# Kernel tuning notes

Hardware: AMD Instinct MI355X
Metric: run time of the kernel (lower is better)

## Reference

```python
import jax, jax.numpy as jnp
import numpy as np

NUM_RELATIONS = 3
NUM_HEADS = 1

N_NODES = 50000
N_EDGES = 300000
D = 256  # in_channels == out_channels == out_channels*num_heads
W_SCALE = 0.02  # realistic init scale; keeps linear-attention normalizer dominated by N_r


def setup_inputs() -> dict:
    key = jax.random.key(0)
    k = jax.random.split(key, 7)
    x = jax.random.normal(k[0], (N_NODES, D), dtype=jnp.float32)
    Wq = jax.random.normal(k[1], (NUM_RELATIONS, D, D * NUM_HEADS), dtype=jnp.float32) * W_SCALE
    Wk = jax.random.normal(k[2], (NUM_RELATIONS, D, D * NUM_HEADS), dtype=jnp.float32) * W_SCALE
    Wv = jax.random.normal(k[3], (NUM_RELATIONS, D, D * NUM_HEADS), dtype=jnp.float32) * W_SCALE
    Whp = jax.random.normal(k[4], (D * NUM_HEADS, D), dtype=jnp.float32) * W_SCALE
    edge_index = jax.random.randint(k[5], (2, N_EDGES), 0, N_NODES, dtype=jnp.int64)
    edge_type = jax.random.randint(k[6], (N_EDGES,), 0, NUM_RELATIONS, dtype=jnp.int64)
    return {"x": x, "Wq": Wq, "Wk": Wk, "Wv": Wv, "Whp": Whp,
            "edge_index": edge_index, "edge_type": edge_type}


def _trans_conv(x, Wq, Wk, Wv, Whp, edge_index, edge_type):
    # x: [N, F], Wq/Wk/Wv: [R, F, H*Dh], Whp: [H*Dh, Dh], edge_index: [2, E]
    row, col = edge_index[0], edge_index[1]
    N = x.shape[0]
    R = Wq.shape[0]
    H = NUM_HEADS
    Dh = Wq.shape[-1] // H
    xr = x[row]  # [E, F] gathered source-node features
    xc = x[col]  # [E, F] gathered target-node features
    x_out = jnp.zeros((N, Dh), dtype=x.dtype)
    for r in range(R):  # small fixed relation loop (structurally distinct weights)
        m = (edge_type == r).astype(x.dtype)  # [E] relation mask (handles ragged sizes)
        Nr = jnp.sum(m)  # number of edges of this relation (the 'N' in full_attention_conv)
        q = (xr @ Wq[r]).reshape(-1, H, Dh)  # [E, H, Dh]
        kk = (xc @ Wk[r]).reshape(-1, H, Dh)
        v = (xc @ Wv[r]).reshape(-1, H, Dh)
        # linear attention (no softmax), masked so only relation-r edges contribute
        kvs = jnp.einsum('e,ehm,ehd->hmd', m, kk, v)        # [H, Dh, Dh]
        num = jnp.einsum('ehm,hmd->ehd', q, kvs) + Nr * v    # [E, H, Dh]
        ks_sum = jnp.einsum('e,ehm->hm', m, kk)              # [H, Dh]
        norm = jnp.einsum('ehm,hm->eh', q, ks_sum)[..., None] + Nr  # [E, H, 1]
        attn = (num / norm).mean(axis=1)                     # [E, Dh] (mean over heads)
        x_out = x_out.at[row].add(m[:, None] * attn)         # scatter-add to source nodes
    return x_out @ Whp  # head projection


def reference(x, Wq, Wk, Wv, Whp, edge_index, edge_type):
    return _trans_conv(x, Wq, Wk, Wv, Whp, edge_index, edge_type)
```

## Files before the change

kernel.cpp:

```cpp
#include <hip/hip_runtime.h>

#define NN 50000
#define EE 300000
#define DD 256
#define RR 3
#define NPAD 50048
#define GS 64
#define SCT (RR * NN)
#define SCB 1024
#define SNB ((SCT + SCB - 1) / SCB)
#define TBLK 3128

using bf16x8 = __attribute__((ext_vector_type(8))) short;
using f32x4  = __attribute__((ext_vector_type(4))) float;

__device__ __forceinline__ float bf2f(unsigned short u) {
    return __uint_as_float(((unsigned)u) << 16);
}
__device__ __forceinline__ unsigned short f2bf(float f) {
    unsigned u = __float_as_uint(f);
    return (unsigned short)((u + 0x7fffu + ((u >> 16) & 1u)) >> 16);
}
__device__ __forceinline__ void gload_lds16(const void* g, void* l) {
    __builtin_amdgcn_global_load_lds(
        (const __attribute__((address_space(1))) unsigned int*)g,
        (__attribute__((address_space(3))) unsigned int*)l, 16, 0, 0);
}

__global__ __launch_bounds__(256) void prep_tc(
    const float* __restrict__ x, const float* __restrict__ Wq,
    const float* __restrict__ Wk, const float* __restrict__ Wv,
    const float* __restrict__ Whp,
    unsigned short* __restrict__ xb, unsigned short* __restrict__ xT,
    unsigned short* __restrict__ Wqb, unsigned short* __restrict__ Wkb,
    unsigned short* __restrict__ Wvb, unsigned short* __restrict__ WhpT)
{
    const int tid = threadIdx.x;
    if (blockIdx.x < TBLK) {
        __shared__ unsigned short t[64][66];
        const int tb = blockIdx.x;
        const int n0 = (tb % 782) * 64, i0 = (tb / 782) * 64;
        const int nl = tid >> 2, c0 = (tid & 3) * 16;
        unsigned short vb[16];
        int n = n0 + nl;
        if (n < NN) {
            const float* src = x + (size_t)n * DD + i0 + c0;
#pragma unroll
            for (int q = 0; q < 16; q += 4) {
                float4 v = *(const float4*)(src + q);
                vb[q] = f2bf(v.x); vb[q + 1] = f2bf(v.y);
                vb[q + 2] = f2bf(v.z); vb[q + 3] = f2bf(v.w);
            }
#pragma unroll
            for (int q = 0; q < 16; q += 4)
                *(ushort4*)(xb + (size_t)n * DD + i0 + c0 + q) =
                    make_ushort4(vb[q], vb[q + 1], vb[q + 2], vb[q + 3]);
        } else {
#pragma unroll
            for (int q = 0; q < 16; q++) vb[q] = 0;
        }
#pragma unroll
        for (int q = 0; q < 16; q++) t[nl][c0 + q] = vb[q];
        __syncthreads();
        const int il = tid >> 2, nc0 = (tid & 3) * 16;
        unsigned short ob[16];
#pragma unroll
        for (int q = 0; q < 16; q++) ob[q] = t[nc0 + q][il];
#pragma unroll
        for (int q = 0; q < 16; q += 4)
            *(ushort4*)(xT + (size_t)(i0 + il) * NPAD + n0 + nc0 + q) =
                make_ushort4(ob[q], ob[q + 1], ob[q + 2], ob[q + 3]);
    } else {
        int t = (blockIdx.x - TBLK) * 256 + tid;
        int slot = t >> 16, o = t & 65535;
        int a = o >> 8, b = o & 255;
        if (slot < 3)       Wqb[(size_t)slot * 65536 + o] = f2bf(Wq[(size_t)slot * 65536 + o]);
        else if (slot < 6)  Wkb[(size_t)(slot - 3) * 65536 + o] = f2bf(Wk[(size_t)(slot - 3) * 65536 + o]);
        else if (slot < 9)  Wvb[(size_t)(slot - 6) * 65536 + o] = f2bf(Wv[(size_t)(slot - 6) * 65536 + o]);
        else if (slot == 9) WhpT[o] = f2bf(Whp[b * 256 + a]);
    }
}

__global__ __launch_bounds__(256) void count_kernel(
    const int* __restrict__ erow, const int* __restrict__ ecol,
    const int* __restrict__ etype, int* __restrict__ c_in,
    int* __restrict__ c_out, int* __restrict__ nr)
{
    __shared__ int lnr[RR];
    if (threadIdx.x < RR) lnr[threadIdx.x] = 0;
    __syncthreads();
    int g = blockIdx.x * blockDim.x + threadIdx.x;
    int stride = gridDim.x * blockDim.x;
    for (int e = g; e < EE; e += stride) {
        int t = etype[e];
        atomicAdd(&c_out[t * NN + erow[e]], 1);
        atomicAdd(&c_in[t * NN + ecol[e]], 1);
        atomicAdd(&lnr[t], 1);
    }
    __syncthreads();
    if (threadIdx.x < RR) atomicAdd(&nr[threadIdx.x], lnr[threadIdx.x]);
}

__global__ __launch_bounds__(256) void scan_reduce(
    const int* __restrict__ cnt, int* __restrict__ bsum)
{
    __shared__ int ws[4];
    const int b = blockIdx.x, tid = threadIdx.x;
    const int i = b * SCB + tid * 4;
    int s = 0;
    if (i < SCT) {
        int4 v = *(const int4*)(cnt + i);
        s = v.x + v.y + v.z + v.w;
    }
#pragma unroll
    for (int off = 32; off; off >>= 1) s += __shfl_down(s, off, 64);
    if ((tid & 63) == 0) ws[tid >> 6] = s;
    __syncthreads();
    if (tid == 0) bsum[b] = ws[0] + ws[1] + ws[2] + ws[3];
}

__global__ __launch_bounds__(256) void scan_top(
    const int* __restrict__ bsum, int* __restrict__ boff, int* __restrict__ offT)
{
    __shared__ int bs[256];
    const int tid = threadIdx.x;
    int v = tid < SNB ? bsum[tid] : 0;
    bs[tid] = v;
    __syncthreads();
    for (int d = 1; d < 256; d <<= 1) {
        int t = (tid >= d) ? bs[tid - d] : 0;
        __syncthreads();
        bs[tid] += t;
        __syncthreads();
    }
    if (tid < SNB) boff[tid] = tid ? bs[tid - 1] : 0;
    if (tid == 255) *offT = bs[255];
}

__global__ __launch_bounds__(256) void scan_bot(
    const int* __restrict__ cnt, const int* __restrict__ boff,
    int* __restrict__ off, int* __restrict__ cur)
{
    __shared__ int bs[256];
    const int b = blockIdx.x, tid = threadIdx.x;
    const int i = b * SCB + tid * 4;
    int4 v = make_int4(0, 0, 0, 0);
    if (i < SCT) v = *(const int4*)(cnt + i);
    int s = v.x + v.y + v.z + v.w;
    bs[tid] = s;
    __syncthreads();
    for (int d = 1; d < 256; d <<= 1) {
        int t = (tid >= d) ? bs[tid - d] : 0;
        __syncthreads();
        bs[tid] += t;
        __syncthreads();
    }
    if (i < SCT) {
        int pre = boff[b] + (tid ? bs[tid - 1] : 0);
        int4 o;
        o.x = pre;
        o.y = pre + v.x;
        o.z = pre + v.x + v.y;
        o.w = pre + v.x + v.y + v.z;
        *(int4*)(off + i) = o;
        *(int4*)(cur + i) = o;
    }
}

__global__ __launch_bounds__(256) void fill_kernel(
    const int* __restrict__ erow, const int* __restrict__ ecol,
    const int* __restrict__ etype, int* __restrict__ cur,
    int* __restrict__ scol)
{
    int e = blockIdx.x * 256 + threadIdx.x;
    if (e < EE) {
        int key = etype[e] * NN + erow[e];
        int p = atomicAdd(&cur[key], 1);
        scol[p] = ecol[e];
    }
}

__global__ __launch_bounds__(256) void wbfxw_kernel(
    const unsigned short* __restrict__ xT, const int* __restrict__ c_in,
    float* __restrict__ xw, unsigned short* __restrict__ wbf)
{
    const int tid = threadIdx.x;
    if (blockIdx.x < 256) {
        __shared__ float red[3][4];
        const int i = blockIdx.x;
        float a0 = 0.f, a1 = 0.f, a2 = 0.f;
        for (int n = tid * 4; n < NN; n += 1024) {
            ushort4 xv = *(const ushort4*)(xT + (size_t)i * NPAD + n);
            int4 w0 = *(const int4*)(c_in + n);
            int4 w1 = *(const int4*)(c_in + NN + n);
            int4 w2 = *(const int4*)(c_in + 2 * NN + n);
            float f0 = bf2f(xv.x), f1 = bf2f(xv.y), f2 = bf2f(xv.z), f3 = bf2f(xv.w);
            a0 += f0 * w0.x + f1 * w0.y + f2 * w0.z + f3 * w0.w;
            a1 += f0 * w1.x + f1 * w1.y + f2 * w1.z + f3 * w1.w;
            a2 += f0 * w2.x + f1 * w2.y + f2 * w2.z + f3 * w2.w;
        }
#pragma unroll
        for (int off = 32; off; off >>= 1) {
            a0 += __shfl_down(a0, off, 64);
            a1 += __shfl_down(a1, off, 64);
            a2 += __shfl_down(a2, off, 64);
        }
        if ((tid & 63) == 0) {
            red[0][tid >> 6] = a0; red[1][tid >> 6] = a1; red[2][tid >> 6] = a2;
        }
        __syncthreads();
        if (tid < 3)
            xw[tid * 256 + i] = red[tid][0] + red[tid][1] + red[tid][2] + red[tid][3];
    } else {
        int t = (blockIdx.x - 256) * 256 + tid;
        if (t < 3 * NPAD) {
            int r = t / NPAD, n = t % NPAD;
            wbf[t] = f2bf(n < NN ? (float)c_in[r * NN + n] : 0.f);
        }
    }
}

__global__ __launch_bounds__(512) void g_kernel(
    const unsigned short* __restrict__ xT, const unsigned short* __restrict__ wbf,
    float* __restrict__ Gp)
{
    __shared__ __align__(16) char ldsA[16384];
    __shared__ __align__(16) char ldsB[16384];
    const int tid = threadIdx.x, lane = tid & 63, wid = tid >> 6;
    const int wr = wid >> 1, wc = wid & 1;
    const int i0 = blockIdx.x * 128, j0 = blockIdx.y * 128;
    const int TPZ = (NPAD / 64 + GS - 1) / GS;
    const int kt0 = blockIdx.z * TPZ;
    const int kt1 = min(NPAD / 64, kt0 + TPZ);

    f32x4 acc[3][2][4];
#pragma unroll
    for (int r = 0; r < 3; r++)
#pragma unroll
        for (int m = 0; m < 2; m++)
#pragma unroll
            for (int n = 0; n < 4; n++) acc[r][m][n] = (f32x4){0.f, 0.f, 0.f, 0.f};

    for (int kt = kt0; kt < kt1; kt++) {
        const int kbyte = kt * 128;
#pragma unroll
        for (int is = 0; is < 2; is++) {
            int lb = is * 8192 + wid * 1024;
            int d = lb + lane * 16;
            int row = d >> 7;
            int sc_ = (d & 127) ^ ((row & 7) << 4);
            gload_lds16((const char*)xT + (size_t)(i0 + row) * (NPAD * 2) + kbyte + sc_, ldsA + lb);
            gload_lds16((const char*)xT + (size_t)(j0 + row) * (NPAD * 2) + kbyte + sc_, ldsB + lb);
        }
        __syncthreads();
#pragma unroll
        for (int kk = 0; kk < 2; kk++) {
            const int cb = kk * 64 + ((lane >> 4) << 4);
            bf16x8 bfr[4];
#pragma unroll
            for (int n = 0; n < 4; n++) {
                int rn = wc * 64 + n * 16 + (lane & 15);
                bfr[n] = *(const bf16x8*)(ldsB + rn * 128 + (cb ^ ((rn & 7) << 4)));
            }
            float au[2][8];
#pragma unroll
            for (int m = 0; m < 2; m++) {
                int row = wr * 32 + m * 16 + (lane & 15);
                bf16x8 ar = *(const bf16x8*)(ldsA + row * 128 + (cb ^ ((row & 7) << 4)));
#pragma unroll
                for (int q = 0; q < 8; q++) au[m][q] = bf2f((unsigned short)ar[q]);
            }
            const int nb = kt * 64 + kk * 32 + ((lane >> 4) << 3);
#pragma unroll
            for (int r = 0; r < 3; r++) {
                bf16x8 wv = *(const bf16x8*)(wbf + (size_t)r * NPAD + nb);
                float wf[8];
#pragma unroll
                for (int q = 0; q < 8; q++) wf[q] = bf2f((unsigned short)wv[q]);
                bf16x8 am[2];
#pragma unroll
                for (int m = 0; m < 2; m++)
#pragma unroll
                    for (int q = 0; q < 8; q++)
                        am[m][q] = (short)f2bf(au[m][q] * wf[q]);
#pragma unroll
                for (int m = 0; m < 2; m++)
#pragma unroll
                    for (int n = 0; n < 4; n++)
                        acc[r][m][n] = __builtin_amdgcn_mfma_f32_16x16x32_bf16(
                            am[m], bfr[n], acc[r][m][n], 0, 0, 0);
            }
        }
        __syncthreads();
    }
    float* base = Gp + ((size_t)blockIdx.z * 4 + blockIdx.x * 2 + blockIdx.y) * 3 * 16384;
#pragma unroll
    for (int r = 0; r < 3; r++)
#pragma unroll
        for (int m = 0; m < 2; m++)
#pragma unroll
            for (int n = 0; n < 4; n++) {
                int col = wc * 64 + n * 16 + (lane & 15);
                int rw0 = wr * 32 + m * 16 + ((lane >> 4) << 2);
#pragma unroll
                for (int reg = 0; reg < 4; reg++)
                    base[r * 16384 + (rw0 + reg) * 128 + col] = acc[r][m][n][reg];
            }
}

__global__ __launch_bounds__(256) void greduce_kernel(
    const float* __restrict__ Gp, unsigned short* __restrict__ Gb)
{
    int gid = blockIdx.x * 256 + threadIdx.x;
    int t = gid >> 14, rem = gid & 16383;
    int r = t % 3, tile = t / 3;
    float s = 0.f;
    for (int z = 0; z < GS; z++)
        s += Gp[(size_t)z * 196608 + ((size_t)tile * 3 + r) * 16384 + rem];
    int i = (tile >> 1) * 128 + (rem >> 7);
    int j = (tile & 1) * 128 + (rem & 127);
    Gb[(size_t)r * 65536 + i * 256 + j] = f2bf(s);
}

__global__ __launch_bounds__(256) void matvec_bf(
    const unsigned short* __restrict__ Mat, const float* __restrict__ v,
    float* __restrict__ y)
{
    __shared__ float vs[256];
    const int b = blockIdx.x;
    const int r = b >> 6, rb = (b & 63) * 4;
    const int tid = threadIdx.x;
    vs[tid] = v[r * 256 + tid];
    __syncthreads();
    const int wid = tid >> 6, lane = tid & 63;
    const int row = rb + wid;
    ushort4 m4 = *(const ushort4*)(Mat + (size_t)r * 65536 + row * 256 + lane * 4);
    float s = bf2f(m4.x) * vs[lane * 4] + bf2f(m4.y) * vs[lane * 4 + 1] +
              bf2f(m4.z) * vs[lane * 4 + 2] + bf2f(m4.w) * vs[lane * 4 + 3];
#pragma unroll
    for (int off = 32; off; off >>= 1) s += __shfl_down(s, off, 64);
    if (lane == 0) y[r * 256 + row] = s;
}

__global__ __launch_bounds__(256) void gather_kernel(
    const unsigned short* __restrict__ xb, const int* __restrict__ scol,
    const int* __restrict__ off, const float* __restrict__ tv,
    const int* __restrict__ c_out, const int* __restrict__ nr,
    unsigned short* __restrict__ Afull)
{
    __shared__ float ts[768];
    __shared__ float nrs[RR];
    const int tid = threadIdx.x;
    for (int k = tid; k < 768; k += 256) ts[k] = tv[k];
    if (tid < RR) nrs[tid] = (float)nr[tid];
    __syncthreads();
    const int wid = tid >> 6, lane = tid & 63;
    const int n = blockIdx.x * 4 + wid;
    if (n >= NN) return;
    ushort4 xv = *(const ushort4*)(xb + (size_t)n * DD + lane * 4);
    float xf[4] = {bf2f(xv.x), bf2f(xv.y), bf2f(xv.z), bf2f(xv.w)};
    float dots[RR];
#pragma unroll
    for (int t = 0; t < RR; t++) {
        float s = xf[0] * ts[t * 256 + lane * 4] + xf[1] * ts[t * 256 + lane * 4 + 1] +
                  xf[2] * ts[t * 256 + lane * 4 + 2] + xf[3] * ts[t * 256 + lane * 4 + 3];
#pragma unroll
        for (int o = 32; o; o >>= 1) s += __shfl_xor(s, o, 64);
        dots[t] = s;
    }
#pragma unroll
    for (int t = 0; t < RR; t++) {
        float nrf = nrs[t];
        float denom = dots[t] + nrf;
        int cnt = c_out[t * NN + n];
        float s2 = cnt ? (float)cnt / denom : 0.f;
        ushort4 o1;
        o1.x = f2bf(s2 * xf[0]); o1.y = f2bf(s2 * xf[1]);
        o1.z = f2bf(s2 * xf[2]); o1.w = f2bf(s2 * xf[3]);
        *(ushort4*)(Afull + (size_t)n * 1536 + t * 256 + lane * 4) = o1;

        float acc[4] = {0.f, 0.f, 0.f, 0.f};
        int b0 = off[t * NN + n], b1 = off[t * NN + n + 1];
        for (int i = b0; i < b1; i++) {
            int col = scol[i];
            ushort4 v = *(const ushort4*)(xb + (size_t)col * DD + lane * 4);
            acc[0] += bf2f(v.x); acc[1] += bf2f(v.y);
            acc[2] += bf2f(v.z); acc[3] += bf2f(v.w);
        }
        float s1 = nrf / denom;
        ushort4 o2;
        o2.x = f2bf(s1 * acc[0]); o2.y = f2bf(s1 * acc[1]);
        o2.z = f2bf(s1 * acc[2]); o2.w = f2bf(s1 * acc[3]);
        *(ushort4*)(Afull + (size_t)n * 1536 + 768 + t * 256 + lane * 4) = o2;
    }
}

template <int MODE, int SWZ>
__global__ __launch_bounds__(256) void gemm_nt(
    const unsigned short* __restrict__ A, int lda,
    const unsigned short* __restrict__ B, int ldb,
    void* __restrict__ Cv, int ldc, int M, int KK,
    size_t sa, size_t sb, size_t sc)
{
    A += (size_t)blockIdx.z * sa;
    B += (size_t)blockIdx.z * sb;
    __shared__ __align__(16) char ldsA[16384];
    __shared__ __align__(16) char ldsB[16384];
    const int tid = threadIdx.x, lane = tid & 63, wid = tid >> 6;
    const int wr = wid >> 1, wc = wid & 1;
    int bx = blockIdx.x;
    if (SWZ) {
        int nwg = gridDim.x, q = nwg >> 3, rem = nwg & 7;
        int xcd = bx & 7, idx = bx >> 3;
        bx = (xcd < rem ? xcd * (q + 1) : rem * (q + 1) + (xcd - rem) * q) + idx;
    }
    const int row0 = bx * 128, col0 = blockIdx.y * 128;

    f32x4 acc[4][4];
#pragma unroll
    for (int m = 0; m < 4; m++)
#pragma unroll
        for (int n = 0; n < 4; n++) acc[m][n] = (f32x4){0.f, 0.f, 0.f, 0.f};

    for (int k0 = 0; k0 < KK; k0 += 64) {
#pragma unroll
        for (int is = 0; is < 4; is++) {
            int lb = is * 4096 + wid * 1024;
            int d = lb + lane * 16;
            int row = d >> 7;
            int sc_ = (d & 127) ^ ((row & 7) << 4);
            int gr = row0 + row; gr = gr < M ? gr : M - 1;
            gload_lds16((const char*)(A + (size_t)gr * lda + k0) + sc_, ldsA + lb);
            int rn = col0 + row;
            gload_lds16((const char*)(B + (size_t)rn * ldb + k0) + sc_, ldsB + lb);
        }
        __syncthreads();
#pragma unroll
        for (int kk = 0; kk < 2; kk++) {
            bf16x8 af[4], bf_[4];
            const int cb = kk * 64 + ((lane >> 4) << 4);
#pragma unroll
            for (int m = 0; m < 4; m++) {
                int row = wr * 64 + m * 16 + (lane & 15);
                af[m] = *(const bf16x8*)(ldsA + row * 128 + (cb ^ ((row & 7) << 4)));
                int rn = wc * 64 + m * 16 + (lane & 15);
                bf_[m] = *(const bf16x8*)(ldsB + rn * 128 + (cb ^ ((rn & 7) << 4)));
            }
#pragma unroll
            for (int m = 0; m < 4; m++)
#pragma unroll
                for (int n = 0; n < 4; n++)
                    acc[m][n] = __builtin_amdgcn_mfma_f32_16x16x32_bf16(
                        af[m], bf_[n], acc[m][n], 0, 0, 0);
        }
        __syncthreads();
    }

#pragma unroll
    for (int m = 0; m < 4; m++) {
#pragma unroll
        for (int reg = 0; reg < 4; reg++) {
            int r = row0 + wr * 64 + m * 16 + ((lane >> 4) << 2) + reg;
            if (r >= M) continue;
#pragma unroll
            for (int n = 0; n < 4; n++) {
                int c = col0 + wc * 64 + n * 16 + (lane & 15);
                float v = acc[m][n][reg];
                if (MODE == 0)
                    ((unsigned short*)Cv)[(size_t)blockIdx.z * sc + (size_t)r * ldc + c] = f2bf(v);
                else
                    ((float*)Cv)[(size_t)blockIdx.z * sc + (size_t)r * ldc + c] = v;
            }
        }
    }
}

extern "C" void kernel_launch(void* const* d_in, const int* in_sizes, int n_in,
                              void* d_out, int out_size, void* d_ws, size_t ws_size,
                              hipStream_t stream)
{
    const float* x   = (const float*)d_in[0];
    const float* Wq  = (const float*)d_in[1];
    const float* Wk  = (const float*)d_in[2];
    const float* Wv  = (const float*)d_in[3];
    const float* Whp = (const float*)d_in[4];
    const int* eidx  = (const int*)d_in[5];
    const int* etyp  = (const int*)d_in[6];
    const int* erow = eidx;
    const int* ecol = eidx + EE;
    float* out = (float*)d_out;

    char* p = (char*)d_ws;
    unsigned short* xb    = (unsigned short*)p; p += (size_t)NN * DD * 2;
    unsigned short* xT    = (unsigned short*)p; p += (size_t)DD * NPAD * 2;
    char*           regB  = p;                  p += (size_t)NN * 1536 * 2;
    unsigned short* Gb    = (unsigned short*)p; p += (size_t)RR * 65536 * 2;
    unsigned short* M1    = (unsigned short*)p; p += (size_t)RR * 65536 * 2;
    unsigned short* Tm    = (unsigned short*)p; p += (size_t)RR * 65536 * 2;
    unsigned short* Bout  = (unsigned short*)p; p += (size_t)256 * 1536 * 2;
    unsigned short* Wqb   = (unsigned short*)p; p += (size_t)RR * 65536 * 2;
    unsigned short* Wkb   = (unsigned short*)p; p += (size_t)RR * 65536 * 2;
    unsigned short* Wvb   = (unsigned short*)p; p += (size_t)RR * 65536 * 2;
    unsigned short* WhpT  = (unsigned short*)p; p += 65536 * 2;
    unsigned short* wbf   = (unsigned short*)p; p += (size_t)RR * NPAD * 2;
    float*          xw    = (float*)p;          p += 768 * 4;
    float*          tv    = (float*)p;          p += 768 * 4;
    int*            c_in  = (int*)p;            p += (size_t)RR * NN * 4;
    int*            c_out = (int*)p;            p += (size_t)RR * NN * 4;
    int*            nr    = (int*)p;            p += 4 * 4;
    int*            off   = (int*)p;            p += (size_t)(RR * NN + 4) * 4;
    int*            cur   = (int*)p;            p += (size_t)RR * NN * 4;
    int*            scol  = (int*)p;            p += (size_t)EE * 4;
    int*            bsum  = (int*)p;            p += SNB * 4;
    int*            boff  = (int*)p;            p += SNB * 4;
    float*          Gp    = (float*)regB;
    unsigned short* Afull = (unsigned short*)regB;

    prep_tc<<<TBLK + 2560, 256, 0, stream>>>(x, Wq, Wk, Wv, Whp, xb, xT, Wqb, Wkb, Wvb, WhpT);
    hipMemsetAsync(c_in, 0, (size_t)(6 * NN + 4) * sizeof(int), stream);
    count_kernel<<<512, 256, 0, stream>>>(erow, ecol, etyp, c_in, c_out, nr);
    scan_reduce<<<SNB, 256, 0, stream>>>(c_out, bsum);
    scan_top<<<1, 256, 0, stream>>>(bsum, boff, off + SCT);
    scan_bot<<<SNB, 256, 0, stream>>>(c_out, boff, off, cur);
    fill_kernel<<<(EE + 255) / 256, 256, 0, stream>>>(erow, ecol, etyp, cur, scol);
    wbfxw_kernel<<<256 + (3 * NPAD + 255) / 256, 256, 0, stream>>>(xT, c_in, xw, wbf);

    gemm_nt<0, 0><<<dim3(2, 2, 3), 256, 0, stream>>>(Wqb, 256, Wkb, 256, M1, 256, 256, 256,
                                                     65536, 65536, 65536);
    gemm_nt<0, 0><<<dim3(2, 2, 3), 256, 0, stream>>>(WhpT, 256, Wvb, 256, Bout + 768, 1536,
                                                     256, 256, 0, 65536, 256);

    g_kernel<<<dim3(2, 2, GS), 512, 0, stream>>>(xT, wbf, Gp);
    greduce_kernel<<<12 * 64, 256, 0, stream>>>(Gp, Gb);

    gemm_nt<0, 0><<<dim3(2, 2, 3), 256, 0, stream>>>(M1, 256, Gb, 256, Tm, 256, 256, 256,
                                                     65536, 65536, 65536);
    gemm_nt<0, 0><<<dim3(2, 2, 3), 256, 0, stream>>>(Bout + 768, 1536, Tm, 256, Bout, 1536,
                                                     256, 256, 256, 65536, 256);
    matvec_bf<<<192, 256, 0, stream>>>(M1, xw, tv);

    gather_kernel<<<(NN + 3) / 4, 256, 0, stream>>>(xb, scol, off, tv, c_out, nr, Afull);

    const int MB = (NN + 127) / 128;
    gemm_nt<1, 1><<<dim3(MB, 2), 256, 0, stream>>>(Afull, 1536, Bout, 1536, out, 256, NN, 1536,
                                                   0, 0, 0);
}
```

Baseline: 320.2 us.

## Replace final projection GEMM with 256x256-tile 1024-thread double-buffered kernel

```diff
diff --git a/kernel.cpp b/kernel.cpp
--- a/kernel.cpp
+++ b/kernel.cpp
@@ -470,6 +470,96 @@
                     ((unsigned short*)Cv)[(size_t)blockIdx.z * sc + (size_t)r * ldc + c] = f2bf(v);
                 else
                     ((float*)Cv)[(size_t)blockIdx.z * sc + (size_t)r * ldc + c] = v;
+            }
+        }
+    }
+}
+
+__global__ __launch_bounds__(1024) void gemm_big(
+    const unsigned short* __restrict__ A, int lda,
+    const unsigned short* __restrict__ B, int ldb,
+    float* __restrict__ C, int ldc, int M, int KK)
+{
+    extern __shared__ __align__(16) char lds[];
+    char* ldsA = lds;
+    char* ldsB = lds + 65536;
+    const int tid = threadIdx.x, lane = tid & 63, wid = tid >> 6;
+    const int wr = wid >> 2, wc = wid & 3;
+    int bx = blockIdx.x;
+    {
+        int nwg = gridDim.x, q = nwg >> 3, rem = nwg & 7;
+        int xcd = bx & 7, idx = bx >> 3;
+        bx = (xcd < rem ? xcd * (q + 1) : rem * (q + 1) + (xcd - rem) * q) + idx;
+    }
+    const int row0 = bx * 256, col0 = blockIdx.y * 256;
+
+    f32x4 acc[4][4];
+#pragma unroll
+    for (int m = 0; m < 4; m++)
+#pragma unroll
+        for (int n = 0; n < 4; n++) acc[m][n] = (f32x4){0.f, 0.f, 0.f, 0.f};
+
+    const int NT = KK / 64;
+    int cur = 0;
+
+#define STAGE_TILE(buf, t)                                                     \
+    {                                                                          \
+        const int k0_ = (t) * 64;                                              \
+        _Pragma("unroll")                                                      \
+        for (int is = 0; is < 2; is++) {                                       \
+            int lb = is * 16384 + wid * 1024;                                  \
+            int d = lb + lane * 16;                                            \
+            int row = d >> 7;                                                  \
+            int sc_ = (d & 127) ^ ((row & 7) << 4);                            \
+            int gr = row0 + row; gr = gr < M ? gr : M - 1;                     \
+            gload_lds16((const char*)(A + (size_t)gr * lda + k0_) + sc_,       \
+                        ldsA + (buf) * 32768 + lb);                            \
+            int rn = col0 + row;                                               \
+            gload_lds16((const char*)(B + (size_t)rn * ldb + k0_) + sc_,       \
+                        ldsB + (buf) * 32768 + lb);                            \
+        }                                                                      \
+    }
+
+    STAGE_TILE(0, 0);
+    __syncthreads();
+
+    for (int t = 0; t < NT; t++) {
+        if (t + 1 < NT) STAGE_TILE(cur ^ 1, t + 1);
+        const char* bA = ldsA + cur * 32768;
+        const char* bB = ldsB + cur * 32768;
+#pragma unroll
+        for (int kk = 0; kk < 2; kk++) {
+            bf16x8 af[4], bf_[4];
+            const int cb = kk * 64 + ((lane >> 4) << 4);
+#pragma unroll
+            for (int m = 0; m < 4; m++) {
+                int row = wr * 64 + m * 16 + (lane & 15);
+                af[m] = *(const bf16x8*)(bA + row * 128 + (cb ^ ((row & 7) << 4)));
+                int rn = wc * 64 + m * 16 + (lane & 15);
+                bf_[m] = *(const bf16x8*)(bB + rn * 128 + (cb ^ ((rn & 7) << 4)));
+            }
+#pragma unroll
+            for (int m = 0; m < 4; m++)
+#pragma unroll
+                for (int n = 0; n < 4; n++)
+                    acc[m][n] = __builtin_amdgcn_mfma_f32_16x16x32_bf16(
+                        af[m], bf_[n], acc[m][n], 0, 0, 0);
+        }
+        __syncthreads();
+        cur ^= 1;
+    }
+#undef STAGE_TILE
+
+#pragma unroll
+    for (int m = 0; m < 4; m++) {
+#pragma unroll
+        for (int reg = 0; reg < 4; reg++) {
+            int r = row0 + wr * 64 + m * 16 + ((lane >> 4) << 2) + reg;
+            if (r >= M) continue;
+#pragma unroll
+            for (int n = 0; n < 4; n++) {
+                int c = col0 + wc * 64 + n * 16 + (lane & 15);
+                C[(size_t)r * ldc + c] = acc[m][n][reg];
             }
         }
     }
@@ -516,6 +606,9 @@
     float*          Gp    = (float*)regB;
     unsigned short* Afull = (unsigned short*)regB;
 
+    hipFuncSetAttribute((const void*)gemm_big,
+                        hipFuncAttributeMaxDynamicSharedMemorySize, 131072);
+
     prep_tc<<<TBLK + 2560, 256, 0, stream>>>(x, Wq, Wk, Wv, Whp, xb, xT, Wqb, Wkb, Wvb, WhpT);
     hipMemsetAsync(c_in, 0, (size_t)(6 * NN + 4) * sizeof(int), stream);
     count_kernel<<<512, 256, 0, stream>>>(erow, ecol, etyp, c_in, c_out, nr);
@@ -541,7 +634,6 @@
 
     gather_kernel<<<(NN + 3) / 4, 256, 0, stream>>>(xb, scol, off, tv, c_out, nr, Afull);
 
-    const int MB = (NN + 127) / 128;
-    gemm_nt<1, 1><<<dim3(MB, 2), 256, 0, stream>>>(Afull, 1536, Bout, 1536, out, 256, NN, 1536,
-                                                   0, 0, 0);
-}
+    const int MB2 = (NN + 255) / 256;
+    gemm_big<<<dim3(MB2, 1), 1024, 131072, stream>>>(Afull, 1536, Bout, 1536, out, 256, NN, 1536);
+}
```

After: 292.1 us. 8.8% less time.

## Fuse per-row scaled x blocks into final GEMM instead of materializing them

Applied to the files above, without the earlier changes.

```diff
diff --git a/kernel.cpp b/kernel.cpp
--- a/kernel.cpp
+++ b/kernel.cpp
@@ -346,7 +346,7 @@
     const unsigned short* __restrict__ xb, const int* __restrict__ scol,
     const int* __restrict__ off, const float* __restrict__ tv,
     const int* __restrict__ c_out, const int* __restrict__ nr,
-    unsigned short* __restrict__ Afull)
+    unsigned short* __restrict__ Ascat, float* __restrict__ s2g)
 {
     __shared__ float ts[768];
     __shared__ float nrs[RR];
@@ -372,13 +372,10 @@
     for (int t = 0; t < RR; t++) {
         float nrf = nrs[t];
         float denom = dots[t] + nrf;
-        int cnt = c_out[t * NN + n];
-        float s2 = cnt ? (float)cnt / denom : 0.f;
-        ushort4 o1;
-        o1.x = f2bf(s2 * xf[0]); o1.y = f2bf(s2 * xf[1]);
-        o1.z = f2bf(s2 * xf[2]); o1.w = f2bf(s2 * xf[3]);
-        *(ushort4*)(Afull + (size_t)n * 1536 + t * 256 + lane * 4) = o1;
-
+        if (lane == 0) {
+            int cnt = c_out[t * NN + n];
+            s2g[(size_t)t * NN + n] = cnt ? (float)cnt / denom : 0.f;
+        }
         float acc[4] = {0.f, 0.f, 0.f, 0.f};
         int b0 = off[t * NN + n], b1 = off[t * NN + n + 1];
         for (int i = b0; i < b1; i++) {
@@ -391,7 +388,7 @@
         ushort4 o2;
         o2.x = f2bf(s1 * acc[0]); o2.y = f2bf(s1 * acc[1]);
         o2.z = f2bf(s1 * acc[2]); o2.w = f2bf(s1 * acc[3]);
-        *(ushort4*)(Afull + (size_t)n * 1536 + 768 + t * 256 + lane * 4) = o2;
+        *(ushort4*)(Ascat + (size_t)n * 768 + t * 256 + lane * 4) = o2;
     }
 }
 
@@ -475,6 +472,135 @@
     }
 }
 
+__global__ __launch_bounds__(512) void gemm_big(
+    const unsigned short* __restrict__ Xb, const unsigned short* __restrict__ As,
+    const unsigned short* __restrict__ Bm, const float* __restrict__ s2g,
+    float* __restrict__ C, int M)
+{
+    extern __shared__ __align__(16) char lds[];
+    char* ldsA = lds;
+    char* ldsB = lds + 32768;
+    float* s2l = (float*)(lds + 98304);
+    const int tid = threadIdx.x, lane = tid & 63, wid = tid >> 6;
+    const int wr = wid >> 2, wc = wid & 3;
+    int bx = blockIdx.x;
+    {
+        int nwg = gridDim.x, q = nwg >> 3, rem = nwg & 7;
+        int xcd = bx & 7, idx = bx >> 3;
+        bx = (xcd < rem ? xcd * (q + 1) : rem * (q + 1) + (xcd - rem) * q) + idx;
+    }
+    const int row0 = bx * 128;
+
+    if (tid < 384) {
+        int rsel = tid >> 7, rr = tid & 127;
+        int gr = row0 + rr; gr = gr < M ? gr : M - 1;
+        s2l[tid] = s2g[(size_t)rsel * NN + gr];
+    }
+
+    f32x4 accO[4][4], acc[4][4];
+#pragma unroll
+    for (int m = 0; m < 4; m++)
+#pragma unroll
+        for (int n = 0; n < 4; n++) {
+            accO[m][n] = (f32x4){0.f, 0.f, 0.f, 0.f};
+            acc[m][n]  = (f32x4){0.f, 0.f, 0.f, 0.f};
+        }
+
+#define STAGE_A(buf, Asrc, ldaE, kE)                                           \
+    { _Pragma("unroll")                                                        \
+      for (int is = 0; is < 2; is++) {                                         \
+          int lb = is * 8192 + wid * 1024;                                     \
+          int d = lb + lane * 16;                                              \
+          int row = d >> 7;                                                    \
+          int sc_ = (d & 127) ^ ((row & 7) << 4);                              \
+          int gr = row0 + row; gr = gr < M ? gr : M - 1;                       \
+          gload_lds16((const char*)((Asrc) + (size_t)gr * (ldaE) + (kE)) + sc_,\
+                      ldsA + (buf) * 16384 + lb); } }
+
+#define STAGE_B(buf, kE)                                                       \
+    { _Pragma("unroll")                                                        \
+      for (int is = 0; is < 4; is++) {                                         \
+          int lb = is * 8192 + wid * 1024;                                     \
+          int d = lb + lane * 16;                                              \
+          int row = d >> 7;                                                    \
+          int sc_ = (d & 127) ^ ((row & 7) << 4);                              \
+          gload_lds16((const char*)(Bm + (size_t)row * 1536 + (kE)) + sc_,     \
+                      ldsB + (buf) * 32768 + lb); } }
+
+#define MFMA_STEP(abuf, bbuf, ACC)                                             \
+    { const char* bA = ldsA + (abuf) * 16384;                                  \
+      const char* bB = ldsB + (bbuf) * 32768;                                  \
+      _Pragma("unroll")                                                        \
+      for (int kk = 0; kk < 2; kk++) {                                         \
+          bf16x8 af[4], bf_[4];                                                \
+          const int cb = kk * 64 + ((lane >> 4) << 4);                         \
+          _Pragma("unroll")                                                    \
+          for (int m = 0; m < 4; m++) {                                        \
+              int row = wr * 64 + m * 16 + (lane & 15);                        \
+              af[m] = *(const bf16x8*)(bA + row * 128 + (cb ^ ((row & 7) << 4)));\
+              int rn = wc * 64 + m * 16 + (lane & 15);                         \
+              bf_[m] = *(const bf16x8*)(bB + rn * 128 + (cb ^ ((rn & 7) << 4)));\
+          }                                                                    \
+          _Pragma("unroll")                                                    \
+          for (int m = 0; m < 4; m++)                                          \
+              _Pragma("unroll")                                                \
+              for (int n = 0; n < 4; n++)                                      \
+                  ACC[m][n] = __builtin_amdgcn_mfma_f32_16x16x32_bf16(         \
+                      af[m], bf_[n], ACC[m][n], 0, 0, 0); } }
+
+    STAGE_A(0, Xb, 256, 0);
+    STAGE_B(0, 0);
+    __syncthreads();
+    int ab = 0, bb = 0;
+
+    for (int r = 0; r < 3; r++) {
+        for (int kt = 0; kt < 4; kt++) {
+            if (kt < 3)      { STAGE_A(ab ^ 1, Xb, 256, (kt + 1) * 64);
+                               STAGE_B(bb ^ 1, r * 256 + (kt + 1) * 64); }
+            else if (r < 2)  { STAGE_A(ab ^ 1, Xb, 256, 0);
+                               STAGE_B(bb ^ 1, (r + 1) * 256); }
+            else             { STAGE_A(ab ^ 1, As, 768, 0);
+                               STAGE_B(bb ^ 1, 768); }
+            MFMA_STEP(ab, bb, acc);
+            __syncthreads();
+            ab ^= 1; bb ^= 1;
+        }
+#pragma unroll
+        for (int m = 0; m < 4; m++) {
+            f32x4 sv = *(const f32x4*)&s2l[r * 128 + wr * 64 + m * 16 + ((lane >> 4) << 2)];
+#pragma unroll
+            for (int n = 0; n < 4; n++) {
+                accO[m][n] += sv * acc[m][n];
+                acc[m][n] = (f32x4){0.f, 0.f, 0.f, 0.f};
+            }
+        }
+    }
+    for (int st = 0; st < 12; st++) {
+        if (st < 11) { STAGE_A(ab ^ 1, As, 768, (st + 1) * 64);
+                       STAGE_B(bb ^ 1, 768 + (st + 1) * 64); }
+        MFMA_STEP(ab, bb, accO);
+        __syncthreads();
+        ab ^= 1; bb ^= 1;
+    }
+#undef STAGE_A
+#undef STAGE_B
+#undef MFMA_STEP
+
+#pragma unroll
+    for (int m = 0; m < 4; m++) {
+#pragma unroll
+        for (int reg = 0; reg < 4; reg++) {
+            int r = row0 + wr * 64 + m * 16 + ((lane >> 4) << 2) + reg;
+            if (r >= M) continue;
+#pragma unroll
+            for (int n = 0; n < 4; n++) {
+                int c = wc * 64 + n * 16 + (lane & 15);
+                C[(size_t)r * 256 + c] = accO[m][n][reg];
+            }
+        }
+    }
+}
+
 extern "C" void kernel_launch(void* const* d_in, const int* in_sizes, int n_in,
                               void* d_out, int out_size, void* d_ws, size_t ws_size,
                               hipStream_t stream)
@@ -493,7 +619,7 @@
     char* p = (char*)d_ws;
     unsigned short* xb    = (unsigned short*)p; p += (size_t)NN * DD * 2;
     unsigned short* xT    = (unsigned short*)p; p += (size_t)DD * NPAD * 2;
-    char*           regB  = p;                  p += (size_t)NN * 1536 * 2;
+    char*           regB  = p;                  p += (size_t)NN * 768 * 2;
     unsigned short* Gb    = (unsigned short*)p; p += (size_t)RR * 65536 * 2;
     unsigned short* M1    = (unsigned short*)p; p += (size_t)RR * 65536 * 2;
     unsigned short* Tm    = (unsigned short*)p; p += (size_t)RR * 65536 * 2;
@@ -505,6 +631,7 @@
     unsigned short* wbf   = (unsigned short*)p; p += (size_t)RR * NPAD * 2;
     float*          xw    = (float*)p;          p += 768 * 4;
     float*          tv    = (float*)p;          p += 768 * 4;
+    float*          s2g   = (float*)p;          p += (size_t)RR * NN * 4;
     int*            c_in  = (int*)p;            p += (size_t)RR * NN * 4;
     int*            c_out = (int*)p;            p += (size_t)RR * NN * 4;
     int*            nr    = (int*)p;            p += 4 * 4;
@@ -514,7 +641,10 @@
     int*            bsum  = (int*)p;            p += SNB * 4;
     int*            boff  = (int*)p;            p += SNB * 4;
     float*          Gp    = (float*)regB;
-    unsigned short* Afull = (unsigned short*)regB;
+    unsigned short* Ascat = (unsigned short*)regB;
+
+    hipFuncSetAttribute((const void*)gemm_big,
+                        hipFuncAttributeMaxDynamicSharedMemorySize, 99840);
 
     prep_tc<<<TBLK + 2560, 256, 0, stream>>>(x, Wq, Wk, Wv, Whp, xb, xT, Wqb, Wkb, Wvb, WhpT);
     hipMemsetAsync(c_in, 0, (size_t)(6 * NN + 4) * sizeof(int), stream);
@@ -539,9 +669,8 @@
                                                      256, 256, 256, 65536, 256);
     matvec_bf<<<192, 256, 0, stream>>>(M1, xw, tv);
 
-    gather_kernel<<<(NN + 3) / 4, 256, 0, stream>>>(xb, scol, off, tv, c_out, nr, Afull);
-
-    const int MB = (NN + 127) / 128;
-    gemm_nt<1, 1><<<dim3(MB, 2), 256, 0, stream>>>(Afull, 1536, Bout, 1536, out, 256, NN, 1536,
-                                                   0, 0, 0);
-}
+    gather_kernel<<<(NN + 3) / 4, 256, 0, stream>>>(xb, scol, off, tv, c_out, nr, Ascat, s2g);
+
+    const int MB2 = (NN + 127) / 128;
+    gemm_big<<<dim3(MB2, 1), 512, 99840, stream>>>(xb, Ascat, Bout, s2g, out, NN);
+}
```

After: 292.4 us. -8.7%, faster.
